# Optimization experiments

Measured on AMD Instinct MI355X. Metric: run time of the kernel, lower is better.

The kernel has to match this reference:

```python
import jax, jax.numpy as jnp
import numpy as np

N = 50000      # num_nodes
NT = 300000    # unique (s, o) pairs
R = 64         # num relations
RP = 16        # latent pseudo-relations
E = 32         # emb_dim
C = 32         # num_classes
LW = 64        # latent MLP width


def setup_inputs() -> dict:
    key = jax.random.key(0)
    ks = jax.random.split(key, 12)
    inp = {
        "s_idx": jax.random.randint(ks[0], (NT,), 0, N, dtype=jnp.int32),
        "o_idx": jax.random.randint(ks[1], (NT,), 0, N, dtype=jnp.int32),
        "nhots": jax.random.uniform(ks[2], (NT, R), dtype=jnp.float32),
        "W1a": jax.random.normal(ks[3], (R, LW), dtype=jnp.float32) * 0.1,
        "b1a": jnp.zeros((LW,), jnp.float32),
        "W1b": jax.random.normal(ks[4], (LW, RP), dtype=jnp.float32) * 0.1,
        "b1b": jnp.zeros((RP,), jnp.float32),
        "W2a": jax.random.normal(ks[5], (R, LW), dtype=jnp.float32) * 0.1,
        "b2a": jnp.zeros((LW,), jnp.float32),
        "W2b": jax.random.normal(ks[6], (LW, RP), dtype=jnp.float32) * 0.1,
        "b2b": jnp.zeros((RP,), jnp.float32),
        "weights1": jax.random.normal(ks[7], (RP, N, E), dtype=jnp.float32) * 0.05,
        "weights2": jax.random.normal(ks[8], (RP, E, C), dtype=jnp.float32) * 0.05,
        "bias1": jnp.zeros((E,), jnp.float32),
        "bias2": jnp.zeros((C,), jnp.float32),
    }
    return inp


def _mlp(x, Wa, ba, Wb, bb):
    # Linear(r, lwidth) -> ReLU -> Linear(lwidth, rp)
    return jax.nn.relu(x @ Wa + ba) @ Wb + bb


def reference(s_idx, o_idx, nhots, W1a, b1a, W1b, b1b, W2a, b2a, W2b, b2b,
              weights1, weights2, bias1, bias2):
    n, rp = N, RP
    e = weights1.shape[2]
    k = jnp.arange(rp, dtype=s_idx.dtype)[:, None]   # [rp, 1]

    # hindices: rows = s (tiled k-major), cols = o * k  -> sparse (n, n*rp)
    hrows = jnp.tile(s_idx, rp)                       # [rp*nt]
    hcols = (o_idx[None, :] * k).reshape(-1)          # [rp*nt]
    # vindices: rows = s * k, cols = o (tiled)        -> sparse (n*rp, n)
    vrows = (s_idx[None, :] * k).reshape(-1)
    vcols = jnp.tile(o_idx, rp)

    # ---- layer 1: latent relation softmax + column-normalized spmm ----
    lat1 = jax.nn.softmax(_mlp(nhots, W1a, b1a, W1b, b1b), axis=1)  # [nt, rp]
    v1 = lat1.T.reshape(-1)                                          # [rp*nt], k-major
    colsum = jax.ops.segment_sum(v1, hcols, num_segments=n * rp)
    v1 = v1 / colsum[hcols]
    # spmm: out[s] += v1 * weights1.view(rp*n, e)[o*k]
    h = jax.ops.segment_sum(v1[:, None] * weights1.reshape(rp * n, e)[hcols],
                            hrows, num_segments=n)                   # [n, e]
    h = jax.nn.relu(h + bias1)

    # ---- layer 2: latent relation softmax + row-normalized spmm ----
    lat2 = jax.nn.softmax(_mlp(nhots, W2a, b2a, W2b, b2b), axis=1)   # [nt, rp]
    v2 = lat2.T.reshape(-1)
    rowsum = jax.ops.segment_sum(v2, vrows, num_segments=n * rp)
    v2 = v2 / rowsum[vrows]
    # spmm: out[s*k] += v2 * h[o]
    h2 = jax.ops.segment_sum(v2[:, None] * h[vcols],
                             vrows, num_segments=n * rp)             # [n*rp, e]
    h2 = h2.reshape(rp, n, e)

    out = jnp.einsum('rhc,rnh->nc', weights2, h2) + bias2            # [n, c]
    return out
```

## Files before the change

kernel.cpp:

```cpp
#include <hip/hip_runtime.h>
#include <hip/hip_bf16.h>

#define DEV_INLINE __device__ __forceinline__

constexpr int kN   = 50000;
constexpr int kNT  = 300000;
constexpr int kR   = 64;
constexpr int kRP  = 16;
constexpr int kE   = 32;
constexpr int kC   = 32;
constexpr int kLW  = 64;
constexpr int kNRP = kN * kRP;
constexpr int kChunks = (kN + 255) / 256;

typedef __attribute__((ext_vector_type(8))) short s8v;
typedef __attribute__((ext_vector_type(4))) float f32x4;

DEV_INLINE short f2bf(float f) {
  union { float f; unsigned u; } v; v.f = f;
  unsigned r = (v.u + 0x7fffu + ((v.u >> 16) & 1u)) >> 16;
  return (short)r;
}
DEV_INLINE float bf2f(short s) {
  union { unsigned u; float f; } v; v.u = ((unsigned)(unsigned short)s) << 16;
  return v.f;
}
DEV_INLINE float bflo(unsigned u) { union { unsigned x; float f; } a; a.x = u << 16;        return a.f; }
DEV_INLINE float bfhi(unsigned u) { union { unsigned x; float f; } a; a.x = u & 0xffff0000u; return a.f; }

union U4S8 { uint4 u; s8v s; };

DEV_INLINE void split8(const float4 A, const float4 B, s8v& hi, s8v& lo) {
  const float f[8] = {A.x, A.y, A.z, A.w, B.x, B.y, B.z, B.w};
  unsigned u[8], l[8];
#pragma unroll
  for (int i = 0; i < 8; i++) { union { float f; unsigned u; } c; c.f = f[i]; u[i] = c.u; }
#pragma unroll
  for (int i = 0; i < 8; i++) {
    union { unsigned u; float f; } t; t.u = u[i] & 0xffff0000u;
    union { float f; unsigned u; } c; c.f = f[i] - t.f; l[i] = c.u;
  }
  U4S8 H, L;
  H.u.x = (u[1] & 0xffff0000u) | (u[0] >> 16);
  H.u.y = (u[3] & 0xffff0000u) | (u[2] >> 16);
  H.u.z = (u[5] & 0xffff0000u) | (u[4] >> 16);
  H.u.w = (u[7] & 0xffff0000u) | (u[6] >> 16);
  L.u.x = (l[1] & 0xffff0000u) | (l[0] >> 16);
  L.u.y = (l[3] & 0xffff0000u) | (l[2] >> 16);
  L.u.z = (l[5] & 0xffff0000u) | (l[4] >> 16);
  L.u.w = (l[7] & 0xffff0000u) | (l[6] >> 16);
  hi = H.s; lo = L.s;
}

__global__ void __launch_bounds__(256)
k_count(const int* __restrict__ s_idx, int* __restrict__ cnt_s) {
  const int e = blockIdx.x * 256 + threadIdx.x;
  if (e < kNT) atomicAdd(&cnt_s[s_idx[e]], 1);
}

__global__ void __launch_bounds__(256)
k_scan_p1(const int* __restrict__ cnt, int* __restrict__ rp, int* __restrict__ bs) {
  __shared__ int ws[4];
  const int tid = threadIdx.x, wave = tid >> 6, lane = tid & 63;
  const int i = blockIdx.x * 256 + tid;
  int v = (i < kN) ? cnt[i] : 0;
  int incl = v;
#pragma unroll
  for (int off = 1; off < 64; off <<= 1) {
    int tmp = __shfl_up(incl, off, 64);
    if (lane >= off) incl += tmp;
  }
  if (lane == 63) ws[wave] = incl;
  __syncthreads();
  int add = 0;
#pragma unroll
  for (int w = 0; w < 4; w++) if (w < wave) add += ws[w];
  incl += add;
  if (i < kN) rp[i + 1] = incl;
  if (tid == 255) bs[blockIdx.x] = incl;
}

__global__ void __launch_bounds__(256)
k_scan_p2(int* __restrict__ bs) {
  __shared__ int ws[4];
  const int tid = threadIdx.x, wave = tid >> 6, lane = tid & 63;
  const int v = (tid < kChunks) ? bs[tid] : 0;
  int incl = v;
#pragma unroll
  for (int off = 1; off < 64; off <<= 1) {
    int tmp = __shfl_up(incl, off, 64);
    if (lane >= off) incl += tmp;
  }
  if (lane == 63) ws[wave] = incl;
  __syncthreads();
  int add = 0;
#pragma unroll
  for (int w = 0; w < 4; w++) if (w < wave) add += ws[w];
  incl += add;
  if (tid < kChunks) bs[tid] = incl - v;
}

__global__ void __launch_bounds__(256)
k_scan_p3(const int* __restrict__ bs, int* __restrict__ rp) {
  const int i = blockIdx.x * 256 + threadIdx.x;
  if (i < kN) rp[i + 1] += bs[blockIdx.x];
  if (blockIdx.x == 0 && threadIdx.x == 0) rp[0] = 0;
}

__global__ void __launch_bounds__(256)
k_scatter(const int* __restrict__ s_idx, const int* __restrict__ o_idx,
          const int* __restrict__ rowptr, int* __restrict__ cursor,
          int* __restrict__ o_csr, int* __restrict__ sslot) {
  const int e = blockIdx.x * 256 + threadIdx.x;
  if (e < kNT) {
    const int s = s_idx[e];
    const int ps = atomicAdd(&cursor[s], 1);
    const int slot = rowptr[s] + ps;
    o_csr[slot] = o_idx[e];
    sslot[e] = slot;
  }
}

__global__ void __launch_bounds__(256)
k_wprep(const float* __restrict__ W1a, const float* __restrict__ W1b,
        const float* __restrict__ W2a, const float* __restrict__ W2b,
        short* __restrict__ Wf) {
  const int tid = threadIdx.x;
  for (int i = tid; i < 8192; i += 256) {
    const int j = i & 7, lane = (i >> 3) & 63, ks = (i >> 9) & 1,
              nt = (i >> 10) & 3, mlp = i >> 12;
    const int p = lane & 15, q8 = (lane >> 4) * 8;
    const float* Wa = mlp ? W2a : W1a;
    const float v = Wa[(ks * 32 + q8 + j) * kLW + nt * 16 + p];
    union { float f; unsigned u; } c; c.f = v;
    const short h = (short)(c.u >> 16);
    Wf[i] = h;
    Wf[8192 + i] = f2bf(v - bf2f(h));
  }
  for (int i = tid; i < 2048; i += 256) {
    const int j = i & 7, lane = (i >> 3) & 63, ks = (i >> 9) & 1, mlp = i >> 10;
    const int p = lane & 15, q8 = (lane >> 4) * 8;
    const float* Wb = mlp ? W2b : W1b;
    const float v = Wb[(ks * 32 + q8 + j) * kRP + p];
    union { float f; unsigned u; } c; c.f = v;
    const short h = (short)(c.u >> 16);
    Wf[16384 + i] = h;
    Wf[18432 + i] = f2bf(v - bf2f(h));
  }
}

__global__ void __launch_bounds__(256)
k_lat(const float* __restrict__ nhots, const short* __restrict__ Wf,
      const float* __restrict__ b1a, const float* __restrict__ b1b,
      const float* __restrict__ b2a, const float* __restrict__ b2b,
      const int* __restrict__ s_idx, const int* __restrict__ o_idx,
      const int* __restrict__ sslot,
      float* __restrict__ lat1o, float* __restrict__ lat2o,
      float* __restrict__ C1, float* __restrict__ R2) {
  __shared__ float sHf[4][16][68];
  const int tid = threadIdx.x;
  const int wave = tid >> 6, lane = tid & 63;
  const int p = lane & 15, q = lane >> 4, q8 = (lane >> 4) * 8;

  const uint4* BaH4 = (const uint4*)(Wf);
  const uint4* BaL4 = (const uint4*)(Wf + 8192);
  const uint4* BbH4 = (const uint4*)(Wf + 16384);
  const uint4* BbL4 = (const uint4*)(Wf + 18432);

  const int w2 = (blockIdx.x * 4 + wave) * 2;

#pragma unroll 1
  for (int mlp = 0; mlp < 2; mlp++) {
    s8v Bh[4][2], Bl[4][2], Bbh[2], Bbl[2];
#pragma unroll
    for (int nt = 0; nt < 4; nt++)
#pragma unroll
      for (int ks = 0; ks < 2; ks++) {
        U4S8 a, b;
        a.u = BaH4[((mlp * 4 + nt) * 2 + ks) * 64 + lane];
        b.u = BaL4[((mlp * 4 + nt) * 2 + ks) * 64 + lane];
        Bh[nt][ks] = a.s; Bl[nt][ks] = b.s;
      }
#pragma unroll
    for (int ks = 0; ks < 2; ks++) {
      U4S8 a, b;
      a.u = BbH4[(mlp * 2 + ks) * 64 + lane];
      b.u = BbL4[(mlp * 2 + ks) * 64 + lane];
      Bbh[ks] = a.s; Bbl[ks] = b.s;
    }
    const float* bA = mlp ? b2a : b1a;
    const float* bB = mlp ? b2b : b1b;
    float bav[4];
#pragma unroll
    for (int nt = 0; nt < 4; nt++) bav[nt] = bA[nt * 16 + p];
    const float bbv = bB[p];
    float* lato = mlp ? lat2o : lat1o;
    const int* nidx = mlp ? s_idx : o_idx;
    float* part = mlp ? R2 : C1;

#pragma unroll 1
    for (int t = 0; t < 2; t++) {
      const int slot = w2 + t;
      if (slot >= kNT / 32) break;
      const int eb = slot * 32;
#pragma unroll 1
      for (int ht = 0; ht < 2; ht++) {
        const int mb = eb + ht * 16;
        int nid[4], sl[4];
#pragma unroll
        for (int reg = 0; reg < 4; reg++) {
          const int m = mb + q * 4 + reg;
          nid[reg] = nidx[m];
          sl[reg]  = sslot[m];
        }
        const float* arow = nhots + (size_t)(mb + p) * kR;
        s8v ah[2], al[2];
#pragma unroll
        for (int ks = 0; ks < 2; ks++) {
          const float4 xa = *(const float4*)(arow + ks * 32 + q8);
          const float4 xb = *(const float4*)(arow + ks * 32 + q8 + 4);
          split8(xa, xb, ah[ks], al[ks]);
        }
        f32x4 acc[4];
#pragma unroll
        for (int nt = 0; nt < 4; nt++) {
          acc[nt] = (f32x4)0.f;
#pragma unroll
          for (int ks = 0; ks < 2; ks++) {
            acc[nt] = __builtin_amdgcn_mfma_f32_16x16x32_bf16(ah[ks], Bh[nt][ks], acc[nt], 0, 0, 0);
            acc[nt] = __builtin_amdgcn_mfma_f32_16x16x32_bf16(ah[ks], Bl[nt][ks], acc[nt], 0, 0, 0);
            acc[nt] = __builtin_amdgcn_mfma_f32_16x16x32_bf16(al[ks], Bh[nt][ks], acc[nt], 0, 0, 0);
          }
        }
#pragma unroll
        for (int nt = 0; nt < 4; nt++)
#pragma unroll
          for (int reg = 0; reg < 4; reg++)
            sHf[wave][q * 4 + reg][nt * 16 + p] = fmaxf(acc[nt][reg] + bav[nt], 0.f);
        const float* hr = &sHf[wave][p][0];
        s8v hh[2], hl[2];
#pragma unroll
        for (int ks = 0; ks < 2; ks++) {
          const float4 xa = *(const float4*)(hr + ks * 32 + q8);
          const float4 xb = *(const float4*)(hr + ks * 32 + q8 + 4);
          split8(xa, xb, hh[ks], hl[ks]);
        }
        f32x4 accB = (f32x4)0.f;
#pragma unroll
        for (int ks = 0; ks < 2; ks++) {
          accB = __builtin_amdgcn_mfma_f32_16x16x32_bf16(hh[ks], Bbh[ks], accB, 0, 0, 0);
          accB = __builtin_amdgcn_mfma_f32_16x16x32_bf16(hh[ks], Bbl[ks], accB, 0, 0, 0);
          accB = __builtin_amdgcn_mfma_f32_16x16x32_bf16(hl[ks], Bbh[ks], accB, 0, 0, 0);
        }
#pragma unroll
        for (int reg = 0; reg < 4; reg++) {
          const float v = accB[reg] + bbv;
          float m = v;
#pragma unroll
          for (int d = 1; d < 16; d <<= 1) m = fmaxf(m, __shfl_xor(m, d));
          const float e = __expf(v - m);
          float sum = e;
#pragma unroll
          for (int d = 1; d < 16; d <<= 1) sum += __shfl_xor(sum, d);
          const float lv = e / sum;
          lato[(size_t)sl[reg] * kRP + p] = lv;
          atomicAdd(&part[(size_t)nid[reg] * kRP + p], lv);
        }
      }
    }
  }
}

__global__ void __launch_bounds__(256)
k_tots(const float* __restrict__ C1, const float* __restrict__ R2,
       float* __restrict__ tots) {
  __shared__ float s0[4], s1[4];
  const int tid = threadIdx.x, wave = tid >> 6, lane = tid & 63;
  float a = 0.f, b = 0.f;
  for (int i = blockIdx.x * 256 + tid; i < kN; i += gridDim.x * 256) {
    a += C1[(size_t)i * kRP];
    b += R2[(size_t)i * kRP];
  }
#pragma unroll
  for (int d = 1; d < 64; d <<= 1) { a += __shfl_xor(a, d); b += __shfl_xor(b, d); }
  if (lane == 0) { s0[wave] = a; s1[wave] = b; }
  __syncthreads();
  if (tid == 0) {
    atomicAdd(&tots[0], s0[0] + s0[1] + s0[2] + s0[3]);
    atomicAdd(&tots[1], s1[0] + s1[1] + s1[2] + s1[3]);
  }
}

__global__ void __launch_bounds__(256)
k_norms(const float* __restrict__ C1, const float* __restrict__ R2,
        const float* __restrict__ tots,
        float* __restrict__ csinv, float* __restrict__ rsinv) {
  const int m = blockIdx.x * 256 + threadIdx.x;
  if (m < kNRP) {
    float cs = (m == 0) ? tots[0] : 0.f;
    float rs = (m == 0) ? tots[1] : 0.f;
#pragma unroll
    for (int k = 1; k < kRP; k++) {
      if (m % k == 0) {
        const int q = m / k;
        if (q < kN) { cs += C1[q * kRP + k]; rs += R2[q * kRP + k]; }
      }
    }
    csinv[m] = (cs != 0.f) ? 1.f / cs : 0.f;
    rsinv[m] = (rs != 0.f) ? 1.f / rs : 0.f;
  }
}

__global__ void __launch_bounds__(256)
k_gbuild(const float* __restrict__ wt1, const float* __restrict__ csinv,
         unsigned* __restrict__ G8u) {
  __shared__ float sT[16][33];
  const int o = blockIdx.x;
  const int tid = threadIdx.x;
#pragma unroll
  for (int half = 0; half < 2; half++) {
    const int e = half * 256 + tid;
    const int k = e >> 5, c = e & 31;
    const int idx = o * k;
    sT[k][c] = csinv[idx] * wt1[(size_t)idx * kE + c];
  }
  __syncthreads();
  const int l = tid >> 2;
  const int c = l >> 1, kh = l & 1;
  const int j0 = (2 * tid) & 7;
  const int k0 = kh * 8 + j0, k1 = k0 + 1;
  const unsigned lo = (unsigned short)f2bf(sT[k0][c]);
  const unsigned hi = (unsigned short)f2bf(sT[k1][c]);
  G8u[(size_t)o * 256 + tid] = lo | (hi << 16);
}

__global__ void __launch_bounds__(256)
k_layer1g(const int* __restrict__ rowptr, const int* __restrict__ o_csr,
          const float* __restrict__ lat1, const uint4* __restrict__ G8,
          const float* __restrict__ bias1, float* __restrict__ h) {
  const int tid = threadIdx.x;
  const int wave = tid >> 6, lane = tid & 63;
  const int c = lane >> 1, kh = lane & 1;
  const float b1 = bias1[c];
  for (int s = blockIdx.x * 4 + wave; s < kN; s += gridDim.x * 4) {
    const int beg = rowptr[s], end = rowptr[s + 1];
    float acc = 0.f;
    int o1 = 0;
    uint4 g0 = (uint4){0, 0, 0, 0};
    float4 la0 = (float4){0.f, 0.f, 0.f, 0.f}, lb0 = la0;
    if (beg < end) {
      const int o0 = o_csr[beg];
      if (beg + 1 < end) o1 = o_csr[beg + 1];
      g0  = G8[(size_t)o0 * 64 + lane];
      la0 = *(const float4*)(lat1 + (size_t)beg * kRP + kh * 8);
      lb0 = *(const float4*)(lat1 + (size_t)beg * kRP + kh * 8 + 4);
    }
    for (int j = beg; j < end; j++) {
      int on = 0;
      uint4 gn = (uint4){0, 0, 0, 0};
      float4 lan = (float4){0.f, 0.f, 0.f, 0.f}, lbn = lan;
      if (j + 2 < end) on = o_csr[j + 2];
      if (j + 1 < end) {
        gn  = G8[(size_t)o1 * 64 + lane];
        lan = *(const float4*)(lat1 + (size_t)(j + 1) * kRP + kh * 8);
        lbn = *(const float4*)(lat1 + (size_t)(j + 1) * kRP + kh * 8 + 4);
      }
      acc = fmaf(la0.x, bflo(g0.x), acc); acc = fmaf(la0.y, bfhi(g0.x), acc);
      acc = fmaf(la0.z, bflo(g0.y), acc); acc = fmaf(la0.w, bfhi(g0.y), acc);
      acc = fmaf(lb0.x, bflo(g0.z), acc); acc = fmaf(lb0.y, bfhi(g0.z), acc);
      acc = fmaf(lb0.z, bflo(g0.w), acc); acc = fmaf(lb0.w, bfhi(g0.w), acc);
      o1 = on; g0 = gn; la0 = lan; lb0 = lbn;
    }
    acc += __shfl_xor(acc, 1);
    if (kh == 0) h[(size_t)s * kE + c] = fmaxf(acc + b1, 0.f);
  }
}

__global__ void __launch_bounds__(256)
k_u(const int* __restrict__ rowptr, const int* __restrict__ o_csr,
    const float* __restrict__ lat2, const float* __restrict__ rsinv,
    const float* __restrict__ h, short* __restrict__ Ub,
    float* __restrict__ pblk) {
  __shared__ float sacc[kE];
  const int tid = threadIdx.x;
  const int wave = tid >> 6, lane = tid & 63;
  const int c = lane & 31, half = lane >> 5;
  if (tid < kE) sacc[tid] = 0.f;
  __syncthreads();
  float hpart = 0.f;
  for (int s = blockIdx.x * 4 + wave; s < kN; s += gridDim.x * 4) {
    float u[8];
#pragma unroll
    for (int kk = 0; kk < 8; kk++) u[kk] = 0.f;
    const int beg = rowptr[s], end = rowptr[s + 1];
    int o1 = 0;
    float hv0 = 0.f;
    float4 la0 = (float4){0.f, 0.f, 0.f, 0.f}, lb0 = la0;
    if (beg < end) {
      const int o0 = o_csr[beg];
      if (beg + 1 < end) o1 = o_csr[beg + 1];
      hv0 = h[(size_t)o0 * kE + c];
      const float4* lp = (const float4*)(lat2 + (size_t)beg * kRP) + half * 2;
      la0 = lp[0]; lb0 = lp[1];
    }
    for (int j = beg; j < end; j++) {
      int on = 0;
      float hvn = 0.f;
      float4 lan = (float4){0.f, 0.f, 0.f, 0.f}, lbn = lan;
      if (j + 2 < end) on = o_csr[j + 2];
      if (j + 1 < end) {
        hvn = h[(size_t)o1 * kE + c];
        const float4* lp = (const float4*)(lat2 + (size_t)(j + 1) * kRP) + half * 2;
        lan = lp[0]; lbn = lp[1];
      }
      u[0] = fmaf(la0.x, hv0, u[0]); u[1] = fmaf(la0.y, hv0, u[1]);
      u[2] = fmaf(la0.z, hv0, u[2]); u[3] = fmaf(la0.w, hv0, u[3]);
      u[4] = fmaf(lb0.x, hv0, u[4]); u[5] = fmaf(lb0.y, hv0, u[5]);
      u[6] = fmaf(lb0.z, hv0, u[6]); u[7] = fmaf(lb0.w, hv0, u[7]);
      o1 = on; hv0 = hvn; la0 = lan; lb0 = lbn;
    }
    if (half == 0) hpart += u[0];
#pragma unroll
    for (int kk = 0; kk < 8; kk++) {
      const int k = half * 8 + kk;
      if (k >= 1)
        Ub[((size_t)s * 15 + (k - 1)) * kE + c] = f2bf(u[kk] * rsinv[s * k]);
    }
  }
  atomicAdd(&sacc[c], hpart);
  __syncthreads();
  if (tid < kE) pblk[(size_t)blockIdx.x * kE + tid] = sacc[tid];
}

__global__ void __launch_bounds__(256)
k_hred(const float* __restrict__ pblk, int nblk, float* __restrict__ hrow0) {
  __shared__ float sacc[kE];
  const int tid = threadIdx.x;
  if (tid < kE) sacc[tid] = 0.f;
  __syncthreads();
  const int total = nblk * kE;
  float r = 0.f;
  for (int i = blockIdx.x * 256 + tid; i < total; i += gridDim.x * 256)
    r += pblk[i];
  atomicAdd(&sacc[tid & 31], r);
  __syncthreads();
  if (tid < kE) atomicAdd(&hrow0[tid], sacc[tid]);
}

__global__ void __launch_bounds__(256)
k_h2(const short* __restrict__ Ub, const float* __restrict__ hrow0,
     const float* __restrict__ rsinv, short* __restrict__ H2) {
  const int tid = threadIdx.x;
  const int g = tid >> 5, c = tid & 31;
  const int n = blockIdx.x * 8 + g;
  const float rs0 = rsinv[0];
  int nm[16];
  nm[0] = 0; nm[1] = 0;
#pragma unroll
  for (int k = 2; k < kRP; k++) nm[k] = n % k;
#pragma unroll
  for (int r = 0; r < kRP; r++) {
    float row = 0.f;
    if (r == 0 && n == 0) row = hrow0[c] * rs0;
#pragma unroll
    for (int k = r + 1; k < kRP; k++) {
      const int target = (k - (r * 50000) % k) % k;
      if (nm[k] == target) {
        const int s = (r * 50000 + n) / k;
        row += bf2f(Ub[((size_t)s * 15 + (k - 1)) * kE + c]);
      }
    }
    H2[((size_t)n * kRP + r) * kE + c] = f2bf(row);
  }
}

__global__ void __launch_bounds__(256)
k_einsum(const short* __restrict__ H2, const float* __restrict__ W2,
         const float* __restrict__ bias2, float* __restrict__ out) {
  __shared__ short sBWh[16 * 2 * 64 * 8];
  __shared__ short sBWl[16 * 2 * 64 * 8];
  const int tid = threadIdx.x;
  for (int i = tid; i < 16384; i += 256) {
    const int j = i & 7, ln = (i >> 3) & 63, nt = (i >> 9) & 1, ks = i >> 10;
    const int pp = ln & 15, qq8 = (ln >> 4) * 8;
    const float v = W2[(ks * 32 + qq8 + j) * 32 + nt * 16 + pp];
    const short h = f2bf(v);
    sBWh[i] = h;
    sBWl[i] = f2bf(v - bf2f(h));
  }
  __syncthreads();
  const int wave = tid >> 6, lane = tid & 63;
  const int p = lane & 15, q = lane >> 4, q8 = q * 8;
  const float bias0 = bias2[p], bias1v = bias2[16 + p];
  for (int tile = blockIdx.x * 4 + wave; tile < kN / 16; tile += gridDim.x * 4) {
    const int mb = tile * 16;
    f32x4 acc0 = (f32x4)0.f, acc1 = (f32x4)0.f;
    const short* arow = H2 + (size_t)(mb + p) * 512 + q8;
#pragma unroll
    for (int ks = 0; ks < 16; ks++) {
      const s8v a   = *(const s8v*)(arow + ks * 32);
      const s8v b0h = *(const s8v*)(sBWh + ((ks * 2 + 0) * 64 + lane) * 8);
      const s8v b0l = *(const s8v*)(sBWl + ((ks * 2 + 0) * 64 + lane) * 8);
      const s8v b1h = *(const s8v*)(sBWh + ((ks * 2 + 1) * 64 + lane) * 8);
      const s8v b1l = *(const s8v*)(sBWl + ((ks * 2 + 1) * 64 + lane) * 8);
      acc0 = __builtin_amdgcn_mfma_f32_16x16x32_bf16(a, b0h, acc0, 0, 0, 0);
      acc0 = __builtin_amdgcn_mfma_f32_16x16x32_bf16(a, b0l, acc0, 0, 0, 0);
      acc1 = __builtin_amdgcn_mfma_f32_16x16x32_bf16(a, b1h, acc1, 0, 0, 0);
      acc1 = __builtin_amdgcn_mfma_f32_16x16x32_bf16(a, b1l, acc1, 0, 0, 0);
    }
#pragma unroll
    for (int reg = 0; reg < 4; reg++) {
      const int n = mb + q * 4 + reg;
      out[(size_t)n * kC + p]      = acc0[reg] + bias0;
      out[(size_t)n * kC + 16 + p] = acc1[reg] + bias1v;
    }
  }
}

extern "C" void kernel_launch(void* const* d_in, const int* in_sizes, int n_in,
                              void* d_out, int out_size, void* d_ws, size_t ws_size,
                              hipStream_t stream) {
  (void)in_sizes; (void)n_in; (void)out_size; (void)ws_size;
  const int* s_idx = (const int*)d_in[0];
  const int* o_idx = (const int*)d_in[1];
  const float* nhots = (const float*)d_in[2];
  const float* W1a = (const float*)d_in[3]; const float* b1a = (const float*)d_in[4];
  const float* W1b = (const float*)d_in[5]; const float* b1b = (const float*)d_in[6];
  const float* W2a = (const float*)d_in[7]; const float* b2a = (const float*)d_in[8];
  const float* W2b = (const float*)d_in[9]; const float* b2b = (const float*)d_in[10];
  const float* wt1 = (const float*)d_in[11]; const float* wt2 = (const float*)d_in[12];
  const float* bias1 = (const float*)d_in[13]; const float* bias2 = (const float*)d_in[14];

  char* ws = (char*)d_ws;
  size_t off = 0;
  auto alloc = [&](size_t bytes) -> char* {
    char* p = ws + off;
    off = (off + bytes + 255) & ~(size_t)255;
    return p;
  };
  char*  z0       = ws;
  int*   cnt_s    = (int*)  alloc((size_t)kN * 4);
  int*   cursor_s = (int*)  alloc((size_t)kN * 4);
  float* tots     = (float*)alloc(8);
  float* hrow0    = (float*)alloc((size_t)kE * 4);
  float* C1       = (float*)alloc((size_t)kNRP * 4);
  float* R2       = (float*)alloc((size_t)kNRP * 4);
  const size_t zbytes = (size_t)((ws + off) - z0);
  short* Wf       = (short*)alloc((size_t)20480 * 2);
  int*   bs_s     = (int*)  alloc((size_t)kChunks * 4);
  int*   rowptr_s = (int*)  alloc((size_t)(kN + 1) * 4);
  float* pblkf    = (float*)alloc((size_t)12500 * kE * 4);
  float* lat2     = (float*)alloc((size_t)kNT * kRP * 4);
  int*   o_csr    = (int*)  alloc((size_t)kNT * 4);
  int*   sslot    = (int*)  alloc((size_t)kNT * 4);
  float* csinv    = (float*)alloc((size_t)kNRP * 4);
  float* rsinv    = (float*)alloc((size_t)kNRP * 4);
  float* hbuf     = (float*)alloc((size_t)kN * kE * 4);
  short* Ub       = (short*)alloc((size_t)kN * 15 * kE * 2);
  char*  Greg     = alloc((size_t)kN * 1024);
  float* lat1     = (float*)Ub;
  unsigned* G8u   = (unsigned*)Greg;
  short* H2       = (short*)Greg;

  hipMemsetAsync(z0, 0, zbytes, stream);

  const dim3 blk(256);
  const int gEdges = (kNT + 255) / 256;
  const int gLat = ((kNT / 32 + 1) / 2 + 3) / 4;

  k_count<<<gEdges, blk, 0, stream>>>(s_idx, cnt_s);
  k_scan_p1<<<kChunks, blk, 0, stream>>>(cnt_s, rowptr_s, bs_s);
  k_scan_p2<<<1, blk, 0, stream>>>(bs_s);
  k_scan_p3<<<kChunks, blk, 0, stream>>>(bs_s, rowptr_s);
  k_scatter<<<gEdges, blk, 0, stream>>>(s_idx, o_idx, rowptr_s, cursor_s,
                                        o_csr, sslot);
  k_wprep<<<1, blk, 0, stream>>>(W1a, W1b, W2a, W2b, Wf);
  k_lat<<<gLat, blk, 0, stream>>>(nhots, Wf, b1a, b1b, b2a, b2b,
                                  s_idx, o_idx, sslot, lat1, lat2, C1, R2);
  k_tots<<<64, blk, 0, stream>>>(C1, R2, tots);
  k_norms<<<(kNRP + 255) / 256, blk, 0, stream>>>(C1, R2, tots, csinv, rsinv);
  k_gbuild<<<kN, blk, 0, stream>>>(wt1, csinv, G8u);
  k_layer1g<<<12500, blk, 0, stream>>>(rowptr_s, o_csr, lat1, (const uint4*)G8u, bias1, hbuf);
  k_u<<<12500, blk, 0, stream>>>(rowptr_s, o_csr, lat2, rsinv, hbuf, Ub, pblkf);
  k_hred<<<50, blk, 0, stream>>>(pblkf, 12500, hrow0);
  k_h2<<<kN / 8, blk, 0, stream>>>(Ub, hrow0, rsinv, H2);
  k_einsum<<<782, blk, 0, stream>>>(H2, wt2, bias2, (float*)d_out);
}
```

Baseline: 557.3 us.

## Fuse H2 construction into einsum kernel via LDS staging

Merges the k_h2 gather kernel and the k_einsum MFMA kernel into one kernel. Each block builds a 64-row tile of H2 in swizzled shared memory and then runs the bf16 split-precision MFMA directly on it. This removes the 51 MB bf16 H2 round trip through global memory and one launch. The W2 hi/lo split moves into the one-time k_wprep pass, and the B fragments are now read from global memory instead of LDS, which may add L2 traffic per tile.

After: 675.8 us. +21.3%, slower.

```diff
diff --git a/kernel.cpp b/kernel.cpp
--- a/kernel.cpp
+++ b/kernel.cpp
@@ -124,7 +124,8 @@
 __global__ void __launch_bounds__(256)
 k_wprep(const float* __restrict__ W1a, const float* __restrict__ W1b,
         const float* __restrict__ W2a, const float* __restrict__ W2b,
-        short* __restrict__ Wf) {
+        const float* __restrict__ wt2,
+        short* __restrict__ Wf, short* __restrict__ Wf2) {
   const int tid = threadIdx.x;
   for (int i = tid; i < 8192; i += 256) {
     const int j = i & 7, lane = (i >> 3) & 63, ks = (i >> 9) & 1,
@@ -146,6 +147,14 @@
     const short h = (short)(c.u >> 16);
     Wf[16384 + i] = h;
     Wf[18432 + i] = f2bf(v - bf2f(h));
+  }
+  for (int i = tid; i < 16384; i += 256) {
+    const int j = i & 7, ln = (i >> 3) & 63, nt = (i >> 9) & 1, ks = i >> 10;
+    const int pp = ln & 15, qq8 = (ln >> 4) * 8;
+    const float v = wt2[(ks * 32 + qq8 + j) * 32 + nt * 16 + pp];
+    const short h = f2bf(v);
+    Wf2[i] = h;
+    Wf2[16384 + i] = f2bf(v - bf2f(h));
   }
 }
 
@@ -448,72 +457,66 @@
 }
 
 __global__ void __launch_bounds__(256)
-k_h2(const short* __restrict__ Ub, const float* __restrict__ hrow0,
-     const float* __restrict__ rsinv, short* __restrict__ H2) {
-  const int tid = threadIdx.x;
-  const int g = tid >> 5, c = tid & 31;
-  const int n = blockIdx.x * 8 + g;
+k_hein(const short* __restrict__ Ub, const float* __restrict__ hrow0,
+       const float* __restrict__ rsinv, const short* __restrict__ Wf2,
+       const float* __restrict__ bias2, float* __restrict__ out) {
+  __shared__ short sH[4][16][512];
+  const int tid = threadIdx.x;
+  const int mb0 = blockIdx.x * 64;
   const float rs0 = rsinv[0];
-  int nm[16];
-  nm[0] = 0; nm[1] = 0;
-#pragma unroll
-  for (int k = 2; k < kRP; k++) nm[k] = n % k;
-#pragma unroll
-  for (int r = 0; r < kRP; r++) {
-    float row = 0.f;
-    if (r == 0 && n == 0) row = hrow0[c] * rs0;
-#pragma unroll
-    for (int k = r + 1; k < kRP; k++) {
-      const int target = (k - (r * 50000) % k) % k;
-      if (nm[k] == target) {
-        const int s = (r * 50000 + n) / k;
-        row += bf2f(Ub[((size_t)s * 15 + (k - 1)) * kE + c]);
+#pragma unroll 1
+  for (int half = 0; half < 8; half++) {
+    const int i = half * 256 + tid;
+    const int row = i >> 5, c = i & 31;
+    const int n = mb0 + row;
+    if (n < kN) {
+      const int sw = (row & 7) << 3;
+      int nm[16];
+      nm[0] = 0; nm[1] = 0;
+#pragma unroll
+      for (int k = 2; k < kRP; k++) nm[k] = n % k;
+#pragma unroll
+      for (int r = 0; r < kRP; r++) {
+        float rowv = 0.f;
+        if (r == 0 && n == 0) rowv = hrow0[c] * rs0;
+#pragma unroll
+        for (int k = r + 1; k < kRP; k++) {
+          const int target = (k - (r * 50000) % k) % k;
+          if (nm[k] == target) {
+            const int s = (r * 50000 + n) / k;
+            rowv += bf2f(Ub[((size_t)s * 15 + (k - 1)) * kE + c]);
+          }
+        }
+        sH[row >> 4][row & 15][(r * 32 + c) ^ sw] = f2bf(rowv);
       }
     }
-    H2[((size_t)n * kRP + r) * kE + c] = f2bf(row);
-  }
-}
-
-__global__ void __launch_bounds__(256)
-k_einsum(const short* __restrict__ H2, const float* __restrict__ W2,
-         const float* __restrict__ bias2, float* __restrict__ out) {
-  __shared__ short sBWh[16 * 2 * 64 * 8];
-  __shared__ short sBWl[16 * 2 * 64 * 8];
-  const int tid = threadIdx.x;
-  for (int i = tid; i < 16384; i += 256) {
-    const int j = i & 7, ln = (i >> 3) & 63, nt = (i >> 9) & 1, ks = i >> 10;
-    const int pp = ln & 15, qq8 = (ln >> 4) * 8;
-    const float v = W2[(ks * 32 + qq8 + j) * 32 + nt * 16 + pp];
-    const short h = f2bf(v);
-    sBWh[i] = h;
-    sBWl[i] = f2bf(v - bf2f(h));
   }
   __syncthreads();
   const int wave = tid >> 6, lane = tid & 63;
   const int p = lane & 15, q = lane >> 4, q8 = q * 8;
+  const int mb = mb0 + wave * 16;
+  if (mb >= kN) return;
+  const int sw = (p & 7) << 3;
   const float bias0 = bias2[p], bias1v = bias2[16 + p];
-  for (int tile = blockIdx.x * 4 + wave; tile < kN / 16; tile += gridDim.x * 4) {
-    const int mb = tile * 16;
-    f32x4 acc0 = (f32x4)0.f, acc1 = (f32x4)0.f;
-    const short* arow = H2 + (size_t)(mb + p) * 512 + q8;
-#pragma unroll
-    for (int ks = 0; ks < 16; ks++) {
-      const s8v a   = *(const s8v*)(arow + ks * 32);
-      const s8v b0h = *(const s8v*)(sBWh + ((ks * 2 + 0) * 64 + lane) * 8);
-      const s8v b0l = *(const s8v*)(sBWl + ((ks * 2 + 0) * 64 + lane) * 8);
-      const s8v b1h = *(const s8v*)(sBWh + ((ks * 2 + 1) * 64 + lane) * 8);
-      const s8v b1l = *(const s8v*)(sBWl + ((ks * 2 + 1) * 64 + lane) * 8);
-      acc0 = __builtin_amdgcn_mfma_f32_16x16x32_bf16(a, b0h, acc0, 0, 0, 0);
-      acc0 = __builtin_amdgcn_mfma_f32_16x16x32_bf16(a, b0l, acc0, 0, 0, 0);
-      acc1 = __builtin_amdgcn_mfma_f32_16x16x32_bf16(a, b1h, acc1, 0, 0, 0);
-      acc1 = __builtin_amdgcn_mfma_f32_16x16x32_bf16(a, b1l, acc1, 0, 0, 0);
-    }
-#pragma unroll
-    for (int reg = 0; reg < 4; reg++) {
-      const int n = mb + q * 4 + reg;
-      out[(size_t)n * kC + p]      = acc0[reg] + bias0;
-      out[(size_t)n * kC + 16 + p] = acc1[reg] + bias1v;
-    }
+  f32x4 acc0 = (f32x4)0.f, acc1 = (f32x4)0.f;
+  const short* arow = &sH[wave][p][0];
+#pragma unroll
+  for (int ks = 0; ks < 16; ks++) {
+    const s8v a   = *(const s8v*)(arow + ((ks * 32 + q8) ^ sw));
+    const s8v b0h = *(const s8v*)(Wf2 + ((ks * 2 + 0) * 64 + lane) * 8);
+    const s8v b0l = *(const s8v*)(Wf2 + 16384 + ((ks * 2 + 0) * 64 + lane) * 8);
+    const s8v b1h = *(const s8v*)(Wf2 + ((ks * 2 + 1) * 64 + lane) * 8);
+    const s8v b1l = *(const s8v*)(Wf2 + 16384 + ((ks * 2 + 1) * 64 + lane) * 8);
+    acc0 = __builtin_amdgcn_mfma_f32_16x16x32_bf16(a, b0h, acc0, 0, 0, 0);
+    acc0 = __builtin_amdgcn_mfma_f32_16x16x32_bf16(a, b0l, acc0, 0, 0, 0);
+    acc1 = __builtin_amdgcn_mfma_f32_16x16x32_bf16(a, b1h, acc1, 0, 0, 0);
+    acc1 = __builtin_amdgcn_mfma_f32_16x16x32_bf16(a, b1l, acc1, 0, 0, 0);
+  }
+#pragma unroll
+  for (int reg = 0; reg < 4; reg++) {
+    const int n = mb + q * 4 + reg;
+    out[(size_t)n * kC + p]      = acc0[reg] + bias0;
+    out[(size_t)n * kC + 16 + p] = acc1[reg] + bias1v;
   }
 }
 
@@ -547,6 +550,7 @@
   float* R2       = (float*)alloc((size_t)kNRP * 4);
   const size_t zbytes = (size_t)((ws + off) - z0);
   short* Wf       = (short*)alloc((size_t)20480 * 2);
+  short* Wf2      = (short*)alloc((size_t)32768 * 2);
   int*   bs_s     = (int*)  alloc((size_t)kChunks * 4);
   int*   rowptr_s = (int*)  alloc((size_t)(kN + 1) * 4);
   float* pblkf    = (float*)alloc((size_t)12500 * kE * 4);
@@ -560,13 +564,13 @@
   char*  Greg     = alloc((size_t)kN * 1024);
   float* lat1     = (float*)Ub;
   unsigned* G8u   = (unsigned*)Greg;
-  short* H2       = (short*)Greg;
 
   hipMemsetAsync(z0, 0, zbytes, stream);
 
   const dim3 blk(256);
   const int gEdges = (kNT + 255) / 256;
   const int gLat = ((kNT / 32 + 1) / 2 + 3) / 4;
+  const int gHein = (kN + 63) / 64;
 
   k_count<<<gEdges, blk, 0, stream>>>(s_idx, cnt_s);
   k_scan_p1<<<kChunks, blk, 0, stream>>>(cnt_s, rowptr_s, bs_s);
@@ -574,7 +578,7 @@
   k_scan_p3<<<kChunks, blk, 0, stream>>>(bs_s, rowptr_s);
   k_scatter<<<gEdges, blk, 0, stream>>>(s_idx, o_idx, rowptr_s, cursor_s,
                                         o_csr, sslot);
-  k_wprep<<<1, blk, 0, stream>>>(W1a, W1b, W2a, W2b, Wf);
+  k_wprep<<<1, blk, 0, stream>>>(W1a, W1b, W2a, W2b, wt2, Wf, Wf2);
   k_lat<<<gLat, blk, 0, stream>>>(nhots, Wf, b1a, b1b, b2a, b2b,
                                   s_idx, o_idx, sslot, lat1, lat2, C1, R2);
   k_tots<<<64, blk, 0, stream>>>(C1, R2, tots);
@@ -583,6 +587,5 @@
   k_layer1g<<<12500, blk, 0, stream>>>(rowptr_s, o_csr, lat1, (const uint4*)G8u, bias1, hbuf);
   k_u<<<12500, blk, 0, stream>>>(rowptr_s, o_csr, lat2, rsinv, hbuf, Ub, pblkf);
   k_hred<<<50, blk, 0, stream>>>(pblkf, 12500, hrow0);
-  k_h2<<<kN / 8, blk, 0, stream>>>(Ub, hrow0, rsinv, H2);
-  k_einsum<<<782, blk, 0, stream>>>(H2, wt2, bias2, (float*)d_out);
-}
+  k_hein<<<gHein, blk, 0, stream>>>(Ub, hrow0, rsinv, Wf2, bias2, (float*)d_out);
+}
```
